# Kernel optimization log

Measured on AMD Instinct MI355X. Metric: run time of the kernel, lower is better.

## Reference

```python
import jax, jax.numpy as jnp
import numpy as np

INDEX_SHIFT = jnp.array([[0, 0], [-1, 0], [1, 0], [0, 1], [-1, 1], [1, 1], [0, -1], [-1, -1], [1, -1]], dtype=jnp.int32)
H, W = 320, 320
C = 32          # embed_dim / feat_channels (hard-coded 32 in module)
NH = 2          # head_num
HD = C // NH    # per-head dim
B, N = 4, 20000


def setup_inputs() -> dict:
    key = jax.random.key(0)
    ks = jax.random.split(key, 8)

    def coords(k):
        # unique (y, x) coords per sample so the coord->index lookup is well defined
        perm = jax.random.permutation(k, H * W)[:N]
        return jnp.stack([perm // W, perm % W], axis=-1).astype(jnp.int32)

    li_coors = jax.vmap(coords)(jax.random.split(ks[0], B))
    ra_coors = jax.vmap(coords)(jax.random.split(ks[1], B))
    li_feats = jax.random.normal(ks[2], (B, N, C), jnp.float32)
    ra_feats = jax.random.normal(ks[3], (B, N, C), jnp.float32)
    pos = jax.random.normal(ks[4], (9, C), jnp.float32) * 0.02

    s = 1.0 / np.sqrt(C)
    out = {"li_bev_feats": li_feats, "li_bev_coors": li_coors,
           "ra_bev_feats": ra_feats, "ra_bev_coors": ra_coors,
           "pos_embedding": pos}
    for i, kk in [(1, ks[5]), (2, ks[6])]:
        k0, k1 = jax.random.split(kk)
        out[f"in_w{i}"] = jax.random.uniform(k0, (3 * C, C), jnp.float32, -s, s)
        out[f"in_b{i}"] = jnp.zeros((3 * C,), jnp.float32)
        out[f"out_w{i}"] = jax.random.uniform(k1, (C, C), jnp.float32, -s, s)
        out[f"out_b{i}"] = jnp.zeros((C,), jnp.float32)
    return out


def _build_kv(q_coors, kv_coors, kv_feats, pos):
    # q_coors, kv_coors: (N,2) int; kv_feats: (N,C)
    n = q_coors.shape[0]
    grid = jnp.full((H * W,), -1, jnp.int32)
    grid = grid.at[kv_coors[:, 0] * W + kv_coors[:, 1]].set(jnp.arange(n, dtype=jnp.int32))
    sc = q_coors[None, :, :] + INDEX_SHIFT[:, None, :]            # (9,N,2)
    valid = (sc[..., 0] >= 0) & (sc[..., 0] < H) & (sc[..., 1] >= 0) & (sc[..., 1] < W)
    flat = jnp.clip(sc[..., 0], 0, H - 1) * W + jnp.clip(sc[..., 1], 0, W - 1)
    sel = jnp.where(valid, grid[flat], -1)                        # (9,N)
    mask = (sel >= 0)[..., None]                                  # (9,N,1)
    g = kv_feats[jnp.maximum(sel, 0)]                             # (9,N,C)
    k = jnp.where(mask, g, 0.0)
    v = jnp.where(mask, g + pos[:, None, :], 0.0)
    return k.transpose(1, 0, 2), v.transpose(1, 0, 2)             # (N,9,C)


def _mha(q, k, v, in_w, in_b, out_w, out_b):
    # q: (N,C); k,v: (N,L,C). torch MultiheadAttention (eval mode, dropout off).
    n, L = k.shape[0], k.shape[1]
    wq, wk, wv = in_w[:C], in_w[C:2 * C], in_w[2 * C:]
    bq, bk, bv = in_b[:C], in_b[C:2 * C], in_b[2 * C:]
    qh = (q @ wq.T + bq).reshape(n, NH, HD)
    kh = (k @ wk.T + bk).reshape(n, L, NH, HD)
    vh = (v @ wv.T + bv).reshape(n, L, NH, HD)
    scores = jnp.einsum('nhd,nlhd->nhl', qh, kh) / np.sqrt(HD)
    attn = jax.nn.softmax(scores, axis=-1)
    o = jnp.einsum('nhl,nlhd->nhd', attn, vh).reshape(n, C)
    return o @ out_w.T + out_b


def _scatter(feats, coors):
    # PointPillarsScatter: place (N,C) feats at (y,x) into a (C,H,W) canvas
    idx = coors[:, 0] * W + coors[:, 1]
    canvas = jnp.zeros((C, H * W), feats.dtype)
    return canvas.at[:, idx].set(feats.T).reshape(C, H, W)


def reference(li_bev_feats, li_bev_coors, ra_bev_feats, ra_bev_coors, pos_embedding,
              in_w1, in_b1, out_w1, out_b1, in_w2, in_b2, out_w2, out_b2):
    def one(li_f, li_c, ra_f, ra_c):
        k, v = _build_kv(li_c, ra_c, ra_f, pos_embedding)
        li_img = _scatter(_mha(li_f, k, v, in_w1, in_b1, out_w1, out_b1), li_c)
        k, v = _build_kv(ra_c, li_c, li_f, pos_embedding)
        ra_img = _scatter(_mha(ra_f, k, v, in_w2, in_b2, out_w2, out_b2), ra_c)
        return li_img, ra_img
    li_imgs, ra_imgs = jax.vmap(one)(li_bev_feats, li_bev_coors, ra_bev_feats, ra_bev_coors)
    return li_imgs, ra_imgs  # each (B, C, H, W)
```

## Files before the change

### kernel.cpp

```cpp
#include <hip/hip_runtime.h>

constexpr int Hh = 320, Ww = 320, Cc = 32, Bb = 4, Nn = 20000;
constexpr int HWp = Hh * Ww;

__global__ __launch_bounds__(256) void prep_k(
    int* __restrict__ grids, const float* __restrict__ pos,
    const float* __restrict__ in_w1, const float* __restrict__ in_w2,
    float* __restrict__ posv) {
  int bx = blockIdx.x;
  if (bx < 800) {
    int i = bx * 256 + threadIdx.x;
    ((int4*)grids)[i] = make_int4(-1, -1, -1, -1);
    return;
  }
  int t = (bx - 800) * 256 + threadIdx.x;
  if (t >= 2 * 9 * Cc) return;
  int dir = t / (9 * Cc);
  int rem = t - dir * 9 * Cc;
  int l = rem / Cc, ch = rem - l * Cc;
  const float* w = (dir == 0 ? in_w1 : in_w2) + (2 * Cc + ch) * Cc;
  const float* pl = pos + l * Cc;
  float acc = 0.f;
  for (int j = 0; j < Cc; j++) acc += pl[j] * w[j];
  posv[t] = acc;
}

constexpr int PROJ_BLOCKS_PER_SB = 313;
constexpr int PROJ_TOTAL = PROJ_BLOCKS_PER_SB * 8;

__global__ __launch_bounds__(256) void project_build_k(
    const float* __restrict__ li_feats, const float* __restrict__ ra_feats,
    const int* __restrict__ li_coors, const int* __restrict__ ra_coors,
    const float* __restrict__ in_w1, const float* __restrict__ in_b1,
    const float* __restrict__ in_w2, const float* __restrict__ in_b2,
    float* __restrict__ Qh, float* __restrict__ Kp, float* __restrict__ Vp,
    int* __restrict__ grids) {
  int bx = blockIdx.x;
  if (bx >= PROJ_TOTAL) {
    int idx = (bx - PROJ_TOTAL) * 256 + threadIdx.x;
    if (idx >= 2 * Bb * Nn) return;
    int src = idx / (Bb * Nn);
    int r = idx - src * (Bb * Nn);
    int b = r / Nn, n = r - b * Nn;
    const int* c = (src == 0 ? li_coors : ra_coors) + ((size_t)b * Nn + n) * 2;
    grids[((size_t)src * Bb + b) * HWp + c[0] * Ww + c[1]] = n;
    return;
  }
  int sb = bx / PROJ_BLOCKS_PER_SB;
  int blk = bx - sb * PROJ_BLOCKS_PER_SB;
  int src = sb >> 2, b = sb & 3;
  __shared__ __align__(16) float wqT[32 * 36];
  __shared__ __align__(16) float wkT[32 * 36];
  __shared__ __align__(16) float wvT[32 * 36];
  __shared__ float bq[Cc];
  const float* wA = src == 0 ? in_w1 : in_w2;
  const float* bA = src == 0 ? in_b1 : in_b2;
  const float* wB = src == 0 ? in_w2 : in_w1;
  int t = threadIdx.x;
  for (int i = t; i < Cc * Cc; i += 256) {
    int c = i >> 5, j = i & 31;
    wqT[j * 36 + c] = wA[i];
    wkT[j * 36 + c] = wB[Cc * Cc + i];
    wvT[j * 36 + c] = wB[2 * Cc * Cc + i];
  }
  if (t < Cc) bq[t] = bA[t];
  __syncthreads();
  int pair = t >> 3, c4 = t & 7;
  int n = blk * 64 + pair * 2;
  if (n >= Nn) return;
  const float* f0 = (src == 0 ? li_feats : ra_feats) + ((size_t)b * Nn + n) * Cc;
  float fv0[32], fv1[32];
  const float4* fp0 = (const float4*)f0;
  const float4* fp1 = (const float4*)(f0 + Cc);
#pragma unroll
  for (int j4 = 0; j4 < 8; j4++) {
    float4 u = fp0[j4];
    fv0[4 * j4 + 0] = u.x; fv0[4 * j4 + 1] = u.y;
    fv0[4 * j4 + 2] = u.z; fv0[4 * j4 + 3] = u.w;
    float4 v = fp1[j4];
    fv1[4 * j4 + 0] = v.x; fv1[4 * j4 + 1] = v.y;
    fv1[4 * j4 + 2] = v.z; fv1[4 * j4 + 3] = v.w;
  }
  const float4* wq4 = (const float4*)wqT;
  const float4* wk4 = (const float4*)wkT;
  const float4* wv4 = (const float4*)wvT;
  float4 bq4 = *(const float4*)(bq + c4 * 4);
  float4 aq0 = bq4, aq1 = bq4;
  float4 ak0 = make_float4(0.f, 0.f, 0.f, 0.f), ak1 = ak0;
  float4 av0 = ak0, av1 = ak0;
#pragma unroll
  for (int j = 0; j < 32; j++) {
    float fj0 = fv0[j], fj1 = fv1[j];
    float4 q4 = wq4[j * 9 + c4];
    float4 k4 = wk4[j * 9 + c4];
    float4 v4 = wv4[j * 9 + c4];
    aq0.x += fj0 * q4.x; aq0.y += fj0 * q4.y; aq0.z += fj0 * q4.z; aq0.w += fj0 * q4.w;
    aq1.x += fj1 * q4.x; aq1.y += fj1 * q4.y; aq1.z += fj1 * q4.z; aq1.w += fj1 * q4.w;
    ak0.x += fj0 * k4.x; ak0.y += fj0 * k4.y; ak0.z += fj0 * k4.z; ak0.w += fj0 * k4.w;
    ak1.x += fj1 * k4.x; ak1.y += fj1 * k4.y; ak1.z += fj1 * k4.z; ak1.w += fj1 * k4.w;
    av0.x += fj0 * v4.x; av0.y += fj0 * v4.y; av0.z += fj0 * v4.z; av0.w += fj0 * v4.w;
    av1.x += fj1 * v4.x; av1.y += fj1 * v4.y; av1.z += fj1 * v4.z; av1.w += fj1 * v4.w;
  }
  int dirq = src, dirkv = 1 - src;
  size_t qbase = (((size_t)dirq * Bb + b) * Nn + n) * Cc + c4 * 4;
  size_t kvbase = (((size_t)dirkv * Bb + b) * Nn + n) * Cc + c4 * 4;
  *(float4*)(Qh + qbase) = aq0;
  *(float4*)(Qh + qbase + Cc) = aq1;
  *(float4*)(Kp + kvbase) = ak0;
  *(float4*)(Kp + kvbase + Cc) = ak1;
  *(float4*)(Vp + kvbase) = av0;
  *(float4*)(Vp + kvbase + Cc) = av1;
}

__global__ __launch_bounds__(256) void attn_k(
    const int* __restrict__ li_coors, const int* __restrict__ ra_coors,
    const int* __restrict__ grids, const float* __restrict__ Qh,
    const float* __restrict__ Kp, const float* __restrict__ Vp,
    const float* __restrict__ posv, const float* __restrict__ in_b1,
    const float* __restrict__ in_b2, const float* __restrict__ out_w1,
    const float* __restrict__ out_b1, const float* __restrict__ out_w2,
    const float* __restrict__ out_b2, float* __restrict__ out_pts) {
  int db = blockIdx.y;
  int dir = db >> 2, b = db & 3;
  __shared__ __align__(16) float ow[Cc * Cc];
  __shared__ __align__(16) float pv[9 * Cc];
  __shared__ float obias[Cc], bk[Cc], bv[Cc];
  const float* owp = dir == 0 ? out_w1 : out_w2;
  const float* obp = dir == 0 ? out_b1 : out_b2;
  const float* ibp = dir == 0 ? in_b1 : in_b2;
  int t = threadIdx.x;
  for (int i = t; i < Cc * Cc; i += 256) ow[i] = owp[i];
  for (int i = t; i < 9 * Cc; i += 256) pv[i] = posv[dir * 9 * Cc + i];
  if (t < Cc) { obias[t] = obp[t]; bk[t] = ibp[Cc + t]; bv[t] = ibp[2 * Cc + t]; }
  __syncthreads();
  int n = blockIdx.x * 256 + t;
  if (n >= Nn) return;
  const int* qc = (dir == 0 ? li_coors : ra_coors) + ((size_t)b * Nn + n) * 2;
  int y = qc[0], x = qc[1];
  const int* g = grids + ((size_t)(1 - dir) * Bb + b) * HWp;
  float4 qh4[8];
  const float4* qp = (const float4*)(Qh + (((size_t)dir * Bb + b) * Nn + n) * Cc);
#pragma unroll
  for (int j = 0; j < 8; j++) qh4[j] = qp[j];
  float sinv0 = 0.f, sinv1 = 0.f;
  const float4* bk4 = (const float4*)bk;
#pragma unroll
  for (int j4 = 0; j4 < 4; j4++) {
    float4 b4 = bk4[j4], q4 = qh4[j4];
    sinv0 += q4.x * b4.x + q4.y * b4.y + q4.z * b4.z + q4.w * b4.w;
  }
#pragma unroll
  for (int j4 = 4; j4 < 8; j4++) {
    float4 b4 = bk4[j4], q4 = qh4[j4];
    sinv1 += q4.x * b4.x + q4.y * b4.y + q4.z * b4.z + q4.w * b4.w;
  }
  sinv0 *= 0.25f;
  sinv1 *= 0.25f;
  const int DY[9] = {0, -1, 1, 0, -1, 1, 0, -1, 1};
  const int DX[9] = {0, 0, 0, 1, 1, 1, -1, -1, -1};
  int sel[9];
  float s0[9], s1[9];
  const float* Kpb = Kp + ((size_t)dir * Bb + b) * Nn * Cc;
#pragma unroll
  for (int l = 0; l < 9; l++) {
    int cy = y + DY[l], cx = x + DX[l];
    int se = -1;
    if ((unsigned)cy < (unsigned)Hh && (unsigned)cx < (unsigned)Ww) se = g[cy * Ww + cx];
    sel[l] = se;
    float d0 = 0.f, d1 = 0.f;
    if (se >= 0) {
      const float4* kp = (const float4*)(Kpb + (size_t)se * Cc);
#pragma unroll
      for (int j4 = 0; j4 < 4; j4++) {
        float4 k4 = kp[j4], q4 = qh4[j4];
        d0 += q4.x * k4.x + q4.y * k4.y + q4.z * k4.z + q4.w * k4.w;
      }
#pragma unroll
      for (int j4 = 4; j4 < 8; j4++) {
        float4 k4 = kp[j4], q4 = qh4[j4];
        d1 += q4.x * k4.x + q4.y * k4.y + q4.z * k4.z + q4.w * k4.w;
      }
    }
    s0[l] = sinv0 + 0.25f * d0;
    s1[l] = sinv1 + 0.25f * d1;
  }
  float m0 = s0[0], m1 = s1[0];
#pragma unroll
  for (int l = 1; l < 9; l++) { m0 = fmaxf(m0, s0[l]); m1 = fmaxf(m1, s1[l]); }
  float sum0 = 0.f, sum1 = 0.f;
#pragma unroll
  for (int l = 0; l < 9; l++) {
    s0[l] = __expf(s0[l] - m0);
    s1[l] = __expf(s1[l] - m1);
    sum0 += s0[l];
    sum1 += s1[l];
  }
  float o[Cc];
#pragma unroll
  for (int j = 0; j < Cc; j++) o[j] = 0.f;
  const float* Vpb = Vp + ((size_t)dir * Bb + b) * Nn * Cc;
  const float4* pv4 = (const float4*)pv;
#pragma unroll
  for (int l = 0; l < 9; l++) {
    int se = sel[l];
    if (se >= 0) {
      const float4* vp = (const float4*)(Vpb + (size_t)se * Cc);
      float w0 = s0[l], w1 = s1[l];
#pragma unroll
      for (int j4 = 0; j4 < 8; j4++) {
        float4 v4 = vp[j4];
        float4 p4 = pv4[l * 8 + j4];
        float w = (j4 < 4) ? w0 : w1;
        o[j4 * 4 + 0] += w * (v4.x + p4.x);
        o[j4 * 4 + 1] += w * (v4.y + p4.y);
        o[j4 * 4 + 2] += w * (v4.z + p4.z);
        o[j4 * 4 + 3] += w * (v4.w + p4.w);
      }
    }
  }
  float r0 = 1.f / sum0, r1 = 1.f / sum1;
#pragma unroll
  for (int j = 0; j < 16; j++) o[j] = o[j] * r0 + bv[j];
#pragma unroll
  for (int j = 16; j < Cc; j++) o[j] = o[j] * r1 + bv[j];
  float* op = out_pts + (((size_t)dir * Bb + b) * Nn + n) * Cc;
  const float4* ow4 = (const float4*)ow;
#pragma unroll
  for (int c0 = 0; c0 < Cc; c0 += 4) {
    float a[4];
#pragma unroll
    for (int u = 0; u < 4; u++) {
      float acc = obias[c0 + u];
#pragma unroll
      for (int j4 = 0; j4 < 8; j4++) {
        float4 w4 = ow4[(c0 + u) * 8 + j4];
        acc += o[j4 * 4 + 0] * w4.x + o[j4 * 4 + 1] * w4.y + o[j4 * 4 + 2] * w4.z +
               o[j4 * 4 + 3] * w4.w;
      }
      a[u] = acc;
    }
    *(float4*)(op + c0) = make_float4(a[0], a[1], a[2], a[3]);
  }
}

__global__ __launch_bounds__(256) void scatter_k(
    const int* __restrict__ grids, const float* __restrict__ out_pts,
    float* __restrict__ out) {
  int db = blockIdx.y;
  int dir = db >> 2, b = db & 3;
  int p = blockIdx.x * 256 + threadIdx.x;
  const int* g = grids + ((size_t)dir * Bb + b) * HWp;
  int se = g[p];
  float* ob = out + (((size_t)dir * Bb + b) * Cc) * HWp + p;
  if (se < 0) {
#pragma unroll
    for (int c = 0; c < Cc; c++) ob[(size_t)c * HWp] = 0.f;
  } else {
    const float4* sp =
        (const float4*)(out_pts + (((size_t)dir * Bb + b) * Nn + se) * Cc);
#pragma unroll
    for (int c4 = 0; c4 < 8; c4++) {
      float4 v = sp[c4];
      ob[(size_t)(c4 * 4 + 0) * HWp] = v.x;
      ob[(size_t)(c4 * 4 + 1) * HWp] = v.y;
      ob[(size_t)(c4 * 4 + 2) * HWp] = v.z;
      ob[(size_t)(c4 * 4 + 3) * HWp] = v.w;
    }
  }
}

extern "C" void kernel_launch(void* const* d_in, const int* in_sizes, int n_in,
                              void* d_out, int out_size, void* d_ws, size_t ws_size,
                              hipStream_t stream) {
  const float* li_feats = (const float*)d_in[0];
  const int* li_coors = (const int*)d_in[1];
  const float* ra_feats = (const float*)d_in[2];
  const int* ra_coors = (const int*)d_in[3];
  const float* pos = (const float*)d_in[4];
  const float* in_w1 = (const float*)d_in[5];
  const float* in_b1 = (const float*)d_in[6];
  const float* out_w1 = (const float*)d_in[7];
  const float* out_b1 = (const float*)d_in[8];
  const float* in_w2 = (const float*)d_in[9];
  const float* in_b2 = (const float*)d_in[10];
  const float* out_w2 = (const float*)d_in[11];
  const float* out_b2 = (const float*)d_in[12];

  char* ws = (char*)d_ws;
  size_t off = 0;
  int* grids = (int*)(ws + off);
  off += (size_t)2 * Bb * HWp * 4;
  float* Qh = (float*)(ws + off);
  off += (size_t)2 * Bb * Nn * Cc * 4;
  float* Kp = (float*)(ws + off);
  off += (size_t)2 * Bb * Nn * Cc * 4;
  float* Vp = (float*)(ws + off);
  off += (size_t)2 * Bb * Nn * Cc * 4;
  float* out_pts = (float*)(ws + off);
  off += (size_t)2 * Bb * Nn * Cc * 4;
  float* posv = (float*)(ws + off);
  off += (size_t)2 * 9 * Cc * 4;

  prep_k<<<803, 256, 0, stream>>>(grids, pos, in_w1, in_w2, posv);
  int build_blocks = (2 * Bb * Nn + 255) / 256;
  project_build_k<<<PROJ_TOTAL + build_blocks, 256, 0, stream>>>(
      li_feats, ra_feats, li_coors, ra_coors, in_w1, in_b1, in_w2, in_b2, Qh, Kp,
      Vp, grids);
  dim3 ga((Nn + 255) / 256, 2 * Bb);
  attn_k<<<ga, 256, 0, stream>>>(li_coors, ra_coors, grids, Qh, Kp, Vp, posv, in_b1,
                                 in_b2, out_w1, out_b1, out_w2, out_b2, out_pts);
  dim3 gs(HWp / 256, 2 * Bb);
  scatter_k<<<gs, 256, 0, stream>>>(grids, out_pts, (float*)d_out);
}
```

Before: 97.71 us.

## Fuse attention into scatter kernel with 4 lanes per pixel; 4-row projection

Attention no longer runs per point and then gets scattered. It now runs inside the scatter kernel, which walks the canvas grid, with four lanes sharing each occupied pixel. Each lane handles 8 channels and combines partial dot products and the output projection through xor shuffles. This removes the out_pts intermediate write and read and one kernel launch. The projection kernel now computes four rows per thread group instead of two, halving its block count and reusing each weight load across more rows. The trade-off is lane divergence at empty pixels: most of the canvas is empty, so many threads only write zeros while their neighbours compute.

```diff
diff --git a/kernel.cpp b/kernel.cpp
--- a/kernel.cpp
+++ b/kernel.cpp
@@ -25,7 +25,7 @@
   posv[t] = acc;
 }
 
-constexpr int PROJ_BLOCKS_PER_SB = 313;
+constexpr int PROJ_BLOCKS_PER_SB = 157;
 constexpr int PROJ_TOTAL = PROJ_BLOCKS_PER_SB * 8;
 
 __global__ __launch_bounds__(256) void project_build_k(
@@ -65,61 +65,65 @@
   }
   if (t < Cc) bq[t] = bA[t];
   __syncthreads();
-  int pair = t >> 3, c4 = t & 7;
-  int n = blk * 64 + pair * 2;
-  if (n >= Nn) return;
-  const float* f0 = (src == 0 ? li_feats : ra_feats) + ((size_t)b * Nn + n) * Cc;
-  float fv0[32], fv1[32];
-  const float4* fp0 = (const float4*)f0;
-  const float4* fp1 = (const float4*)(f0 + Cc);
-#pragma unroll
-  for (int j4 = 0; j4 < 8; j4++) {
-    float4 u = fp0[j4];
-    fv0[4 * j4 + 0] = u.x; fv0[4 * j4 + 1] = u.y;
-    fv0[4 * j4 + 2] = u.z; fv0[4 * j4 + 3] = u.w;
-    float4 v = fp1[j4];
-    fv1[4 * j4 + 0] = v.x; fv1[4 * j4 + 1] = v.y;
-    fv1[4 * j4 + 2] = v.z; fv1[4 * j4 + 3] = v.w;
-  }
+  int quad = t >> 3, c4 = t & 7;
+  int n0 = blk * 128 + quad * 4;
+  if (n0 + 4 > Nn) n0 = Nn - 4;
+  const float* f = (src == 0 ? li_feats : ra_feats) + ((size_t)b * Nn + n0) * Cc;
   const float4* wq4 = (const float4*)wqT;
   const float4* wk4 = (const float4*)wkT;
   const float4* wv4 = (const float4*)wvT;
   float4 bq4 = *(const float4*)(bq + c4 * 4);
-  float4 aq0 = bq4, aq1 = bq4;
-  float4 ak0 = make_float4(0.f, 0.f, 0.f, 0.f), ak1 = ak0;
-  float4 av0 = ak0, av1 = ak0;
-#pragma unroll
-  for (int j = 0; j < 32; j++) {
-    float fj0 = fv0[j], fj1 = fv1[j];
-    float4 q4 = wq4[j * 9 + c4];
-    float4 k4 = wk4[j * 9 + c4];
-    float4 v4 = wv4[j * 9 + c4];
-    aq0.x += fj0 * q4.x; aq0.y += fj0 * q4.y; aq0.z += fj0 * q4.z; aq0.w += fj0 * q4.w;
-    aq1.x += fj1 * q4.x; aq1.y += fj1 * q4.y; aq1.z += fj1 * q4.z; aq1.w += fj1 * q4.w;
-    ak0.x += fj0 * k4.x; ak0.y += fj0 * k4.y; ak0.z += fj0 * k4.z; ak0.w += fj0 * k4.w;
-    ak1.x += fj1 * k4.x; ak1.y += fj1 * k4.y; ak1.z += fj1 * k4.z; ak1.w += fj1 * k4.w;
-    av0.x += fj0 * v4.x; av0.y += fj0 * v4.y; av0.z += fj0 * v4.z; av0.w += fj0 * v4.w;
-    av1.x += fj1 * v4.x; av1.y += fj1 * v4.y; av1.z += fj1 * v4.z; av1.w += fj1 * v4.w;
+  float4 aq[4], ak[4], av[4];
+#pragma unroll
+  for (int i = 0; i < 4; i++) {
+    aq[i] = bq4;
+    ak[i] = make_float4(0.f, 0.f, 0.f, 0.f);
+    av[i] = make_float4(0.f, 0.f, 0.f, 0.f);
+  }
+#pragma unroll
+  for (int j4 = 0; j4 < 8; j4++) {
+    float fjs[4][4];
+#pragma unroll
+    for (int i = 0; i < 4; i++) {
+      float4 v = ((const float4*)(f + i * Cc))[j4];
+      fjs[i][0] = v.x; fjs[i][1] = v.y; fjs[i][2] = v.z; fjs[i][3] = v.w;
+    }
+#pragma unroll
+    for (int u = 0; u < 4; u++) {
+      int j = j4 * 4 + u;
+      float4 q4 = wq4[j * 9 + c4];
+      float4 k4 = wk4[j * 9 + c4];
+      float4 v4 = wv4[j * 9 + c4];
+#pragma unroll
+      for (int i = 0; i < 4; i++) {
+        float fj = fjs[i][u];
+        aq[i].x += fj * q4.x; aq[i].y += fj * q4.y;
+        aq[i].z += fj * q4.z; aq[i].w += fj * q4.w;
+        ak[i].x += fj * k4.x; ak[i].y += fj * k4.y;
+        ak[i].z += fj * k4.z; ak[i].w += fj * k4.w;
+        av[i].x += fj * v4.x; av[i].y += fj * v4.y;
+        av[i].z += fj * v4.z; av[i].w += fj * v4.w;
+      }
+    }
   }
   int dirq = src, dirkv = 1 - src;
-  size_t qbase = (((size_t)dirq * Bb + b) * Nn + n) * Cc + c4 * 4;
-  size_t kvbase = (((size_t)dirkv * Bb + b) * Nn + n) * Cc + c4 * 4;
-  *(float4*)(Qh + qbase) = aq0;
-  *(float4*)(Qh + qbase + Cc) = aq1;
-  *(float4*)(Kp + kvbase) = ak0;
-  *(float4*)(Kp + kvbase + Cc) = ak1;
-  *(float4*)(Vp + kvbase) = av0;
-  *(float4*)(Vp + kvbase + Cc) = av1;
-}
-
-__global__ __launch_bounds__(256) void attn_k(
-    const int* __restrict__ li_coors, const int* __restrict__ ra_coors,
+  size_t qbase = (((size_t)dirq * Bb + b) * Nn + n0) * Cc + c4 * 4;
+  size_t kvbase = (((size_t)dirkv * Bb + b) * Nn + n0) * Cc + c4 * 4;
+#pragma unroll
+  for (int i = 0; i < 4; i++) {
+    *(float4*)(Qh + qbase + i * Cc) = aq[i];
+    *(float4*)(Kp + kvbase + i * Cc) = ak[i];
+    *(float4*)(Vp + kvbase + i * Cc) = av[i];
+  }
+}
+
+__global__ __launch_bounds__(256) void scatter_attn_k(
     const int* __restrict__ grids, const float* __restrict__ Qh,
     const float* __restrict__ Kp, const float* __restrict__ Vp,
     const float* __restrict__ posv, const float* __restrict__ in_b1,
     const float* __restrict__ in_b2, const float* __restrict__ out_w1,
     const float* __restrict__ out_b1, const float* __restrict__ out_w2,
-    const float* __restrict__ out_b2, float* __restrict__ out_pts) {
+    const float* __restrict__ out_b2, float* __restrict__ out) {
   int db = blockIdx.y;
   int dir = db >> 2, b = db & 3;
   __shared__ __align__(16) float ow[Cc * Cc];
@@ -133,139 +137,120 @@
   for (int i = t; i < 9 * Cc; i += 256) pv[i] = posv[dir * 9 * Cc + i];
   if (t < Cc) { obias[t] = obp[t]; bk[t] = ibp[Cc + t]; bv[t] = ibp[2 * Cc + t]; }
   __syncthreads();
-  int n = blockIdx.x * 256 + t;
-  if (n >= Nn) return;
-  const int* qc = (dir == 0 ? li_coors : ra_coors) + ((size_t)b * Nn + n) * 2;
-  int y = qc[0], x = qc[1];
-  const int* g = grids + ((size_t)(1 - dir) * Bb + b) * HWp;
-  float4 qh4[8];
-  const float4* qp = (const float4*)(Qh + (((size_t)dir * Bb + b) * Nn + n) * Cc);
-#pragma unroll
-  for (int j = 0; j < 8; j++) qh4[j] = qp[j];
-  float sinv0 = 0.f, sinv1 = 0.f;
-  const float4* bk4 = (const float4*)bk;
-#pragma unroll
-  for (int j4 = 0; j4 < 4; j4++) {
-    float4 b4 = bk4[j4], q4 = qh4[j4];
-    sinv0 += q4.x * b4.x + q4.y * b4.y + q4.z * b4.z + q4.w * b4.w;
-  }
-#pragma unroll
-  for (int j4 = 4; j4 < 8; j4++) {
-    float4 b4 = bk4[j4], q4 = qh4[j4];
-    sinv1 += q4.x * b4.x + q4.y * b4.y + q4.z * b4.z + q4.w * b4.w;
-  }
-  sinv0 *= 0.25f;
-  sinv1 *= 0.25f;
-  const int DY[9] = {0, -1, 1, 0, -1, 1, 0, -1, 1};
-  const int DX[9] = {0, 0, 0, 1, 1, 1, -1, -1, -1};
-  int sel[9];
-  float s0[9], s1[9];
-  const float* Kpb = Kp + ((size_t)dir * Bb + b) * Nn * Cc;
-#pragma unroll
-  for (int l = 0; l < 9; l++) {
-    int cy = y + DY[l], cx = x + DX[l];
-    int se = -1;
-    if ((unsigned)cy < (unsigned)Hh && (unsigned)cx < (unsigned)Ww) se = g[cy * Ww + cx];
-    sel[l] = se;
-    float d0 = 0.f, d1 = 0.f;
-    if (se >= 0) {
-      const float4* kp = (const float4*)(Kpb + (size_t)se * Cc);
-#pragma unroll
-      for (int j4 = 0; j4 < 4; j4++) {
-        float4 k4 = kp[j4], q4 = qh4[j4];
-        d0 += q4.x * k4.x + q4.y * k4.y + q4.z * k4.z + q4.w * k4.w;
-      }
-#pragma unroll
-      for (int j4 = 4; j4 < 8; j4++) {
-        float4 k4 = kp[j4], q4 = qh4[j4];
-        d1 += q4.x * k4.x + q4.y * k4.y + q4.z * k4.z + q4.w * k4.w;
-      }
-    }
-    s0[l] = sinv0 + 0.25f * d0;
-    s1[l] = sinv1 + 0.25f * d1;
-  }
-  float m0 = s0[0], m1 = s1[0];
-#pragma unroll
-  for (int l = 1; l < 9; l++) { m0 = fmaxf(m0, s0[l]); m1 = fmaxf(m1, s1[l]); }
-  float sum0 = 0.f, sum1 = 0.f;
-#pragma unroll
-  for (int l = 0; l < 9; l++) {
-    s0[l] = __expf(s0[l] - m0);
-    s1[l] = __expf(s1[l] - m1);
-    sum0 += s0[l];
-    sum1 += s1[l];
-  }
-  float o[Cc];
-#pragma unroll
-  for (int j = 0; j < Cc; j++) o[j] = 0.f;
-  const float* Vpb = Vp + ((size_t)dir * Bb + b) * Nn * Cc;
-  const float4* pv4 = (const float4*)pv;
-#pragma unroll
-  for (int l = 0; l < 9; l++) {
-    int se = sel[l];
-    if (se >= 0) {
-      const float4* vp = (const float4*)(Vpb + (size_t)se * Cc);
-      float w0 = s0[l], w1 = s1[l];
-#pragma unroll
-      for (int j4 = 0; j4 < 8; j4++) {
-        float4 v4 = vp[j4];
-        float4 p4 = pv4[l * 8 + j4];
-        float w = (j4 < 4) ? w0 : w1;
-        o[j4 * 4 + 0] += w * (v4.x + p4.x);
-        o[j4 * 4 + 1] += w * (v4.y + p4.y);
-        o[j4 * 4 + 2] += w * (v4.z + p4.z);
-        o[j4 * 4 + 3] += w * (v4.w + p4.w);
-      }
-    }
-  }
-  float r0 = 1.f / sum0, r1 = 1.f / sum1;
-#pragma unroll
-  for (int j = 0; j < 16; j++) o[j] = o[j] * r0 + bv[j];
-#pragma unroll
-  for (int j = 16; j < Cc; j++) o[j] = o[j] * r1 + bv[j];
-  float* op = out_pts + (((size_t)dir * Bb + b) * Nn + n) * Cc;
-  const float4* ow4 = (const float4*)ow;
-#pragma unroll
-  for (int c0 = 0; c0 < Cc; c0 += 4) {
-    float a[4];
-#pragma unroll
-    for (int u = 0; u < 4; u++) {
-      float acc = obias[c0 + u];
-#pragma unroll
-      for (int j4 = 0; j4 < 8; j4++) {
-        float4 w4 = ow4[(c0 + u) * 8 + j4];
-        acc += o[j4 * 4 + 0] * w4.x + o[j4 * 4 + 1] * w4.y + o[j4 * 4 + 2] * w4.z +
-               o[j4 * 4 + 3] * w4.w;
-      }
-      a[u] = acc;
-    }
-    *(float4*)(op + c0) = make_float4(a[0], a[1], a[2], a[3]);
-  }
-}
-
-__global__ __launch_bounds__(256) void scatter_k(
-    const int* __restrict__ grids, const float* __restrict__ out_pts,
-    float* __restrict__ out) {
-  int db = blockIdx.y;
-  int dir = db >> 2, b = db & 3;
-  int p = blockIdx.x * 256 + threadIdx.x;
-  const int* g = grids + ((size_t)dir * Bb + b) * HWp;
-  int se = g[p];
+  int sub = t & 3;
+  int p = blockIdx.x * 64 + (t >> 2);
+  const int* gq = grids + ((size_t)dir * Bb + b) * HWp;
+  int se = gq[p];
+  float outv[8];
+  if (se >= 0) {
+    int cb = sub * 8;
+    const float* Qb = Qh + (((size_t)dir * Bb + b) * Nn + se) * Cc + cb;
+    float qh[8];
+    {
+      float4 a = ((const float4*)Qb)[0], c = ((const float4*)Qb)[1];
+      qh[0] = a.x; qh[1] = a.y; qh[2] = a.z; qh[3] = a.w;
+      qh[4] = c.x; qh[5] = c.y; qh[6] = c.z; qh[7] = c.w;
+    }
+    float pb = 0.f;
+#pragma unroll
+    for (int k = 0; k < 8; k++) pb += qh[k] * bk[cb + k];
+    pb += __shfl_xor(pb, 1);
+    int y = p / Ww, x = p - (p / Ww) * Ww;
+    const int* gkv = grids + ((size_t)(1 - dir) * Bb + b) * HWp;
+    const int DY[9] = {0, -1, 1, 0, -1, 1, 0, -1, 1};
+    const int DX[9] = {0, 0, 0, 1, 1, 1, -1, -1, -1};
+    int sel[9];
+    float s[9];
+    const float* Kpb = Kp + ((size_t)dir * Bb + b) * Nn * Cc;
+#pragma unroll
+    for (int l = 0; l < 9; l++) {
+      int cy = y + DY[l], cx = x + DX[l];
+      int seL = -1;
+      if ((unsigned)cy < (unsigned)Hh && (unsigned)cx < (unsigned)Ww)
+        seL = gkv[cy * Ww + cx];
+      sel[l] = seL;
+      float d = 0.f;
+      if (seL >= 0) {
+        const float* kp = Kpb + (size_t)seL * Cc + cb;
+        float4 a = ((const float4*)kp)[0], c = ((const float4*)kp)[1];
+        d = qh[0] * a.x + qh[1] * a.y + qh[2] * a.z + qh[3] * a.w +
+            qh[4] * c.x + qh[5] * c.y + qh[6] * c.z + qh[7] * c.w;
+      }
+      d += __shfl_xor(d, 1);
+      s[l] = 0.25f * (pb + d);
+    }
+    float m = s[0];
+#pragma unroll
+    for (int l = 1; l < 9; l++) m = fmaxf(m, s[l]);
+    float sum = 0.f;
+#pragma unroll
+    for (int l = 0; l < 9; l++) {
+      s[l] = __expf(s[l] - m);
+      sum += s[l];
+    }
+    float o8[8];
+#pragma unroll
+    for (int k = 0; k < 8; k++) o8[k] = 0.f;
+    const float* Vpb = Vp + ((size_t)dir * Bb + b) * Nn * Cc;
+#pragma unroll
+    for (int l = 0; l < 9; l++) {
+      int seL = sel[l];
+      if (seL >= 0) {
+        const float* vp = Vpb + (size_t)seL * Cc + cb;
+        float4 a = ((const float4*)vp)[0], c = ((const float4*)vp)[1];
+        float w = s[l];
+        const float* pvl = pv + l * Cc + cb;
+        o8[0] += w * (a.x + pvl[0]); o8[1] += w * (a.y + pvl[1]);
+        o8[2] += w * (a.z + pvl[2]); o8[3] += w * (a.w + pvl[3]);
+        o8[4] += w * (c.x + pvl[4]); o8[5] += w * (c.y + pvl[5]);
+        o8[6] += w * (c.z + pvl[6]); o8[7] += w * (c.w + pvl[7]);
+      }
+    }
+    float r = 1.f / sum;
+#pragma unroll
+    for (int k = 0; k < 8; k++) o8[k] = o8[k] * r + bv[cb + k];
+    float a1[8], a2[8], a3[8];
+#pragma unroll
+    for (int k = 0; k < 8; k++) a1[k] = __shfl_xor(o8[k], 1);
+#pragma unroll
+    for (int k = 0; k < 8; k++) a2[k] = __shfl_xor(o8[k], 2);
+#pragma unroll
+    for (int k = 0; k < 8; k++) a3[k] = __shfl_xor(a1[k], 2);
+#pragma unroll
+    for (int cc = 0; cc < 8; cc++) {
+      int c = cb + cc;
+      float acc = obias[c];
+      const float* owr = ow + c * Cc;
+      {
+        int jb = sub;
+#pragma unroll
+        for (int k = 0; k < 8; k++) acc += o8[k] * owr[jb * 8 + k];
+      }
+      {
+        int jb = sub ^ 1;
+#pragma unroll
+        for (int k = 0; k < 8; k++) acc += a1[k] * owr[jb * 8 + k];
+      }
+      {
+        int jb = sub ^ 2;
+#pragma unroll
+        for (int k = 0; k < 8; k++) acc += a2[k] * owr[jb * 8 + k];
+      }
+      {
+        int jb = sub ^ 3;
+#pragma unroll
+        for (int k = 0; k < 8; k++) acc += a3[k] * owr[jb * 8 + k];
+      }
+      outv[cc] = acc;
+    }
+  } else {
+#pragma unroll
+    for (int cc = 0; cc < 8; cc++) outv[cc] = 0.f;
+  }
   float* ob = out + (((size_t)dir * Bb + b) * Cc) * HWp + p;
-  if (se < 0) {
-#pragma unroll
-    for (int c = 0; c < Cc; c++) ob[(size_t)c * HWp] = 0.f;
-  } else {
-    const float4* sp =
-        (const float4*)(out_pts + (((size_t)dir * Bb + b) * Nn + se) * Cc);
-#pragma unroll
-    for (int c4 = 0; c4 < 8; c4++) {
-      float4 v = sp[c4];
-      ob[(size_t)(c4 * 4 + 0) * HWp] = v.x;
-      ob[(size_t)(c4 * 4 + 1) * HWp] = v.y;
-      ob[(size_t)(c4 * 4 + 2) * HWp] = v.z;
-      ob[(size_t)(c4 * 4 + 3) * HWp] = v.w;
-    }
+#pragma unroll
+  for (int cc = 0; cc < 8; cc++) {
+    ob[(size_t)(sub * 8 + cc) * HWp] = outv[cc];
   }
 }
 
@@ -296,8 +281,6 @@
   off += (size_t)2 * Bb * Nn * Cc * 4;
   float* Vp = (float*)(ws + off);
   off += (size_t)2 * Bb * Nn * Cc * 4;
-  float* out_pts = (float*)(ws + off);
-  off += (size_t)2 * Bb * Nn * Cc * 4;
   float* posv = (float*)(ws + off);
   off += (size_t)2 * 9 * Cc * 4;
 
@@ -306,9 +289,8 @@
   project_build_k<<<PROJ_TOTAL + build_blocks, 256, 0, stream>>>(
       li_feats, ra_feats, li_coors, ra_coors, in_w1, in_b1, in_w2, in_b2, Qh, Kp,
       Vp, grids);
-  dim3 ga((Nn + 255) / 256, 2 * Bb);
-  attn_k<<<ga, 256, 0, stream>>>(li_coors, ra_coors, grids, Qh, Kp, Vp, posv, in_b1,
-                                 in_b2, out_w1, out_b1, out_w2, out_b2, out_pts);
-  dim3 gs(HWp / 256, 2 * Bb);
-  scatter_k<<<gs, 256, 0, stream>>>(grids, out_pts, (float*)d_out);
-}
+  dim3 gs(HWp / 64, 2 * Bb);
+  scatter_attn_k<<<gs, 256, 0, stream>>>(grids, Qh, Kp, Vp, posv, in_b1, in_b2,
+                                         out_w1, out_b1, out_w2, out_b2,
+                                         (float*)d_out);
+}
```

Result: slower. 170.8 us (+74.9%).
